# Performance work log

Measured on AMD Instinct MI355X. Metric: run time of the kernel, lower is better.

## Reference

```python
import jax, jax.numpy as jnp
import numpy as np

D_MODEL = 512; D_INNER = 1024; D_SSM = 512; D_STATE = 16; DT_RANK = 32; D_CONV = 4
BETA = 0.0; ALPHA = 1.0  # module defaults: no momentum -> vanilla Longhorn scan
B = 8; L = 2048


def dwconv_silu(x, w, b):
    # x: (B, C, L), w: (C, 1, K); torch F.conv1d(padding='same') with K=4 pads (left=1, right=2)
    y = jax.lax.conv_general_dilated(
        x, w, window_strides=(1,), padding=[(1, 2)],
        dimension_numbers=('NCH', 'OIH', 'NCH'), feature_group_count=x.shape[1])
    y = y + b[None, :, None]
    return y * jax.nn.sigmoid(y)


def longhorn_scan(u, q, k, dt, D_skip, t_bias):
    # u, dt: (B, D, L); q, k: (B, N, L). Longhorn online-learner SSM with momentum velocity.
    delta = jax.nn.softplus(dt + t_bias[None, :, None])           # (B, D, L)
    k2 = jnp.sum(k * k, axis=1, keepdims=True)                    # (B, 1, L)
    eps = delta / (1.0 + delta * k2)                              # implicit-update step size

    def step(carry, inp):
        S, v = carry                                              # (B, D, N) each
        eps_t, u_t, k_t, q_t = inp                                # (B,D),(B,D),(B,N),(B,N)
        g = eps_t[:, :, None] * (u_t[:, :, None] - S * k_t[:, None, :]) * k_t[:, None, :]
        v = BETA * v + ALPHA * g                                  # momentum velocity
        S = S + v
        y_t = jnp.einsum('bdn,bn->bd', S, q_t)
        return (S, v), y_t

    Bq, Dm, _ = u.shape
    S0 = jnp.zeros((Bq, Dm, q.shape[1]), u.dtype)
    xs = (jnp.moveaxis(eps, 2, 0), jnp.moveaxis(u, 2, 0),
          jnp.moveaxis(k, 2, 0), jnp.moveaxis(q, 2, 0))
    _, ys = jax.lax.scan(step, (S0, S0), xs)                      # ys: (L, B, D)
    return jnp.moveaxis(ys, 0, 2) + D_skip[None, :, None] * u    # (B, D, L)


def setup_inputs() -> dict:
    key = jax.random.key(0)
    ks = jax.random.split(key, 12)
    s = lambda k, shape, sc: jax.random.normal(k, shape, jnp.float32) * sc
    dt0 = jnp.exp(jax.random.uniform(ks[8], (D_SSM,), jnp.float32,
                                     float(np.log(1e-3)), float(np.log(1e-1))))
    b_dt = jnp.log(jnp.expm1(dt0))  # inv-softplus init as in torch module
    return {
        'hidden_states': s(ks[0], (B, L, D_MODEL), 1.0),
        'W_in': s(ks[1], (D_INNER, D_MODEL), 0.02),
        'conv_x_w': s(ks[2], (D_SSM, 1, D_CONV), 0.3),
        'conv_x_b': s(ks[3], (D_SSM,), 0.02),
        'conv_z_w': s(ks[4], (D_SSM, 1, D_CONV), 0.3),
        'conv_z_b': s(ks[5], (D_SSM,), 0.02),
        'W_xproj': s(ks[6], (DT_RANK + 2 * D_STATE, D_SSM), 0.05),
        'W_dt': s(ks[7], (D_SSM, DT_RANK), DT_RANK ** -0.5),
        'b_dt': b_dt,
        'D_skip': jnp.ones((D_SSM,), jnp.float32),
        'W_out': s(ks[9], (D_MODEL, D_INNER), 0.02),
    }


def reference(hidden_states, W_in, conv_x_w, conv_x_b, conv_z_w, conv_z_b,
              W_xproj, W_dt, b_dt, D_skip, W_out):
    xz = jnp.einsum('bld,ed->ble', hidden_states, W_in)           # (B, L, d_inner)
    xz = jnp.swapaxes(xz, 1, 2)                                   # (B, d_inner, L)
    x, z = xz[:, :D_SSM], xz[:, D_SSM:]
    x = dwconv_silu(x, conv_x_w, conv_x_b)
    z = dwconv_silu(z, conv_z_w, conv_z_b)
    x_dbl = jnp.einsum('bdl,ed->bel', x, W_xproj)                 # (B, r+2N, L)
    dt_low = x_dbl[:, :DT_RANK]
    k = x_dbl[:, DT_RANK:DT_RANK + D_STATE]
    q = x_dbl[:, DT_RANK + D_STATE:]
    dt = jnp.einsum('dr,brl->bdl', W_dt, dt_low)                  # (B, d_ssm, L)
    y = longhorn_scan(x, q, k, dt, D_skip, b_dt)                  # (B, d_ssm, L)
    y = jnp.concatenate([y, z], axis=1)                           # (B, d_inner, L)
    y = jnp.swapaxes(y, 1, 2)                                     # (B, L, d_inner)
    return jnp.einsum('ble,de->bld', y, W_out)                    # (B, L, d_model)
```

## Files before the change

kernel.cpp:

```cpp
#include <hip/hip_runtime.h>
#include <hip/hip_bf16.h>
#include <math.h>

#define BB 8
#define LL 2048
#define DMODEL 512
#define DINNER 1024
#define DSSM 512
#define NST 16
#define DTR 32
#define NXD 640
#define CCH 64
#define LC (LL / CCH)
#define BDN (BB * DSSM * NST)
#define CLW 8

typedef short short8 __attribute__((ext_vector_type(8)));
typedef float f32x4 __attribute__((ext_vector_type(4)));

__device__ __forceinline__ unsigned short f2bf(float f) {
  unsigned u = __float_as_uint(f);
  u += 0x7FFFu + ((u >> 16) & 1u);
  return (unsigned short)(u >> 16);
}
__device__ __forceinline__ float bf2f(unsigned short s) {
  return __uint_as_float(((unsigned)s) << 16);
}

__device__ __forceinline__ void gload16(const void* g, void* l) {
  __builtin_amdgcn_global_load_lds(
      (const __attribute__((address_space(1))) void*)g,
      (__attribute__((address_space(3))) void*)l, 16, 0, 0);
}

template<bool OUTBF>
__global__ __launch_bounds__(256) void gemm_bf16(
    const unsigned short* __restrict__ Ab,
    const unsigned short* __restrict__ Wb,
    void* __restrict__ Cout, int K, int NBN) {
  __shared__ unsigned short tA[128 * 64];
  __shared__ unsigned short tW[128 * 64];
  const int tid = threadIdx.x;
  const int ln = tid & 63;
  const int wv = tid >> 6;
  const int wr = wv >> 1, wc = wv & 1;
  const int lr = ln & 15, kc = ln >> 4;

  const int nwg = gridDim.x;
  const int q = nwg >> 3;
  const int bid = blockIdx.x;
  const int wg = (bid & 7) * q + (bid >> 3);
  const int mblk = wg / NBN, nblk = wg % NBN;
  const size_t m0 = (size_t)mblk * 128, n0 = (size_t)nblk * 128;

  f32x4 acc[4][4];
#pragma unroll
  for (int m = 0; m < 4; ++m)
#pragma unroll
    for (int n = 0; n < 4; ++n)
#pragma unroll
      for (int j = 0; j < 4; ++j) acc[m][n][j] = 0.f;

  const int wbase = (tid & 0xC0) << 4;

  for (int k0 = 0; k0 < K; k0 += 64) {
#pragma unroll
    for (int it = 0; it < 4; ++it) {
      const int gi = it * 256 + tid;
      const int r = gi >> 3, s = gi & 7, g = s ^ (r & 7);
      const size_t off = (m0 + r) * (size_t)K + (size_t)(k0 + g * 8);
      gload16(Ab + off, (char*)tA + it * 4096 + wbase);
    }
#pragma unroll
    for (int it = 0; it < 4; ++it) {
      const int gi = it * 256 + tid;
      const int r = gi >> 3, s = gi & 7, g = s ^ (r & 7);
      const size_t off = (n0 + r) * (size_t)K + (size_t)(k0 + g * 8);
      gload16(Wb + off, (char*)tW + it * 4096 + wbase);
    }
    __syncthreads();

    short8 alo[4], ahi[4], wlo[4], whi[4];
#pragma unroll
    for (int m = 0; m < 4; ++m) {
      const int ra = wr * 64 + m * 16 + lr;
      const int sl = kc ^ (ra & 7);
      const char* base = (const char*)tA + ra * 128;
      alo[m] = *(const short8*)(base + sl * 16);
      ahi[m] = *(const short8*)(base + (sl ^ 4) * 16);
    }
#pragma unroll
    for (int n = 0; n < 4; ++n) {
      const int rb = wc * 64 + n * 16 + lr;
      const int sl = kc ^ (rb & 7);
      const char* base = (const char*)tW + rb * 128;
      wlo[n] = *(const short8*)(base + sl * 16);
      whi[n] = *(const short8*)(base + (sl ^ 4) * 16);
    }
#pragma unroll
    for (int m = 0; m < 4; ++m)
#pragma unroll
      for (int n = 0; n < 4; ++n) {
        acc[m][n] = __builtin_amdgcn_mfma_f32_16x16x32_bf16(alo[m], wlo[n], acc[m][n], 0, 0, 0);
        acc[m][n] = __builtin_amdgcn_mfma_f32_16x16x32_bf16(ahi[m], whi[n], acc[m][n], 0, 0, 0);
      }
    __syncthreads();
  }

  const int ldc = NBN * 128;
#pragma unroll
  for (int m = 0; m < 4; ++m) {
    const size_t row0 = m0 + wr * 64 + m * 16 + kc * 4;
#pragma unroll
    for (int n = 0; n < 4; ++n) {
      const size_t col = n0 + wc * 64 + n * 16 + lr;
#pragma unroll
      for (int j = 0; j < 4; ++j) {
        if (OUTBF)
          ((unsigned short*)Cout)[(row0 + j) * (size_t)ldc + col] = f2bf(acc[m][n][j]);
        else
          ((float*)Cout)[(row0 + j) * (size_t)ldc + col] = acc[m][n][j];
      }
    }
  }
}

__global__ __launch_bounds__(256) void cvt_kernel(const float* __restrict__ in,
    unsigned short* __restrict__ o, int n4) {
  int i = blockIdx.x * 256 + threadIdx.x;
  const int str = gridDim.x * 256;
  for (; i < n4; i += str) {
    const float4 v = ((const float4*)in)[i];
    ushort4 h;
    h.x = f2bf(v.x); h.y = f2bf(v.y); h.z = f2bf(v.z); h.w = f2bf(v.w);
    ((ushort4*)o)[i] = h;
  }
}

__global__ __launch_bounds__(256) void weff_kernel(
    const float* __restrict__ W_dt, const float* __restrict__ W_xproj,
    unsigned short* __restrict__ WcatB) {
  const int c = blockIdx.x * 256 + threadIdx.x;
  const int r0 = blockIdx.y;
  float v;
  if (r0 < 512) {
    float acc = 0.f;
#pragma unroll
    for (int r = 0; r < 32; r++)
      acc = fmaf(W_dt[r0 * 32 + r], W_xproj[r * 512 + c], acc);
    v = acc;
  } else if (r0 < 544) {
    v = W_xproj[(r0 - 480) * 512 + c];
  } else {
    v = 0.f;
  }
  WcatB[(size_t)r0 * 512 + c] = f2bf(v);
}

__global__ __launch_bounds__(256) void conv_silu_kernel(
    const unsigned short* __restrict__ xzB,
    const float* __restrict__ cxw, const float* __restrict__ cxb,
    const float* __restrict__ czw, const float* __restrict__ czb,
    unsigned short* __restrict__ xcB, unsigned short* __restrict__ yB) {
  const int c = blockIdx.x * 256 + threadIdx.x;
  const int l0 = blockIdx.y * CLW;
  const int b = blockIdx.z;
  float w0, w1, w2, w3, bias;
  if (c < DSSM) {
    w0 = cxw[c * 4 + 0]; w1 = cxw[c * 4 + 1]; w2 = cxw[c * 4 + 2]; w3 = cxw[c * 4 + 3];
    bias = cxb[c];
  } else {
    const int cz = c - DSSM;
    w0 = czw[cz * 4 + 0]; w1 = czw[cz * 4 + 1]; w2 = czw[cz * 4 + 2]; w3 = czw[cz * 4 + 3];
    bias = czb[cz];
  }
  const unsigned short* base = xzB + ((size_t)b * LL + l0) * DINNER + c;
  float v[CLW + 3];
  v[0] = (l0 > 0) ? bf2f(base[-(int)DINNER]) : 0.f;
#pragma unroll
  for (int i = 0; i <= CLW + 1; i++) {
    const int l = l0 + i;
    v[i + 1] = (l < LL) ? bf2f(base[(size_t)i * DINNER]) : 0.f;
  }
#pragma unroll
  for (int j = 0; j < CLW; j++) {
    float a = bias;
    a = fmaf(v[j + 0], w0, a);
    a = fmaf(v[j + 1], w1, a);
    a = fmaf(v[j + 2], w2, a);
    a = fmaf(v[j + 3], w3, a);
    const float y = a / (1.f + expf(-a));
    const size_t bl = (size_t)b * LL + l0 + j;
    if (c < DSSM)
      xcB[bl * DSSM + c] = f2bf(y);
    else
      yB[bl * DINNER + c] = f2bf(y);
  }
}

__global__ __launch_bounds__(256) void dteps2_kernel(
    const float* __restrict__ xdbl2, const float* __restrict__ b_dt,
    float* __restrict__ eps) {
  const int half = blockIdx.x;
  const size_t row = blockIdx.y;
  const int d = half * 256 + threadIdx.x;
  const float* rp = xdbl2 + row * NXD;
  float k2 = 0.f;
#pragma unroll
  for (int n = 0; n < 16; n++) { const float kv = rp[512 + n]; k2 = fmaf(kv, kv, k2); }
  const float dt = rp[d] + b_dt[d];
  const float delta = (dt > 20.f) ? dt : log1pf(expf(dt));
  eps[row * DSSM + d] = delta / (1.f + delta * k2);
}

__global__ __launch_bounds__(256) void scan_passA(
    const float* __restrict__ eps, const unsigned short* __restrict__ xcB,
    const float* __restrict__ xdbl2,
    float* __restrict__ Ach, float* __restrict__ Bch) {
  const int d = blockIdx.x * 256 + threadIdx.x;
  const int b = blockIdx.y, ch = blockIdx.z;
  const size_t bl0 = (size_t)b * LL + (size_t)ch * LC;
  const float* ep = eps + bl0 * DSSM + d;
  const unsigned short* up = xcB + bl0 * DSSM + d;
  const float* kq = xdbl2 + bl0 * NXD + 512;
  float A[16], S[16];
#pragma unroll
  for (int n = 0; n < 16; n++) { A[n] = 1.f; S[n] = 0.f; }
#pragma unroll 2
  for (int j = 0; j < LC; j++) {
    const float e = ep[(size_t)j * DSSM];
    const float u = bf2f(up[(size_t)j * DSSM]);
    const float* kj = kq + j * NXD;
#pragma unroll
    for (int n = 0; n < 16; n++) {
      const float k = kj[n];
      const float t0 = e * k;
      const float a = fmaf(-t0, k, 1.f);
      A[n] *= a;
      S[n] = fmaf(S[n], a, t0 * u);
    }
  }
  const size_t base = (size_t)ch * BDN + (((size_t)b * DSSM + d) << 4);
#pragma unroll
  for (int n4 = 0; n4 < 4; n4++) {
    ((float4*)(Ach + base))[n4] =
        make_float4(A[4 * n4], A[4 * n4 + 1], A[4 * n4 + 2], A[4 * n4 + 3]);
    ((float4*)(Bch + base))[n4] =
        make_float4(S[4 * n4], S[4 * n4 + 1], S[4 * n4 + 2], S[4 * n4 + 3]);
  }
}

__global__ __launch_bounds__(256) void scan_passB(
    const float* __restrict__ Ach, const float* __restrict__ Bch,
    float* __restrict__ S0) {
  const size_t i = (size_t)blockIdx.x * 256 + threadIdx.x;
  float S = 0.f;
  for (int ch = 0; ch < CCH; ch++) {
    const size_t off = (size_t)ch * BDN + i;
    const float a = Ach[off];
    const float bv = Bch[off];
    S0[off] = S;
    S = fmaf(S, a, bv);
  }
}

__global__ __launch_bounds__(256) void scan_passC(
    const float* __restrict__ eps, const unsigned short* __restrict__ xcB,
    const float* __restrict__ xdbl2, const float* __restrict__ D_skip,
    const float* __restrict__ S0, unsigned short* __restrict__ yB) {
  const int d = blockIdx.x * 256 + threadIdx.x;
  const int b = blockIdx.y, ch = blockIdx.z;
  const size_t bl0 = (size_t)b * LL + (size_t)ch * LC;
  const float* ep = eps + bl0 * DSSM + d;
  const unsigned short* up = xcB + bl0 * DSSM + d;
  const float* kq = xdbl2 + bl0 * NXD + 512;
  unsigned short* yp = yB + bl0 * DINNER + d;
  const float Dv = D_skip[d];
  const size_t base = (size_t)ch * BDN + (((size_t)b * DSSM + d) << 4);
  float S[16];
#pragma unroll
  for (int n4 = 0; n4 < 4; n4++) {
    const float4 v = ((const float4*)(S0 + base))[n4];
    S[4 * n4 + 0] = v.x; S[4 * n4 + 1] = v.y;
    S[4 * n4 + 2] = v.z; S[4 * n4 + 3] = v.w;
  }
#pragma unroll 2
  for (int j = 0; j < LC; j++) {
    const float e = ep[(size_t)j * DSSM];
    const float u = bf2f(up[(size_t)j * DSSM]);
    const float* kj = kq + j * NXD;
#pragma unroll
    for (int n = 0; n < 16; n++) {
      const float k = kj[n];
      const float t0 = e * k;
      const float a = fmaf(-t0, k, 1.f);
      S[n] = fmaf(S[n], a, t0 * u);
    }
    float y0 = 0.f, y1 = 0.f, y2 = 0.f, y3 = 0.f;
#pragma unroll
    for (int n = 0; n < 16; n += 4) {
      y0 = fmaf(S[n + 0], kj[16 + n + 0], y0);
      y1 = fmaf(S[n + 1], kj[16 + n + 1], y1);
      y2 = fmaf(S[n + 2], kj[16 + n + 2], y2);
      y3 = fmaf(S[n + 3], kj[16 + n + 3], y3);
    }
    const float yv = fmaf(Dv, u, (y0 + y1) + (y2 + y3));
    yp[(size_t)j * DINNER] = f2bf(yv);
  }
}

extern "C" void kernel_launch(void* const* d_in, const int* in_sizes, int n_in,
                              void* d_out, int out_size, void* d_ws, size_t ws_size,
                              hipStream_t stream) {
  const float* hidden  = (const float*)d_in[0];
  const float* W_in    = (const float*)d_in[1];
  const float* cxw     = (const float*)d_in[2];
  const float* cxb     = (const float*)d_in[3];
  const float* czw     = (const float*)d_in[4];
  const float* czb     = (const float*)d_in[5];
  const float* W_xproj = (const float*)d_in[6];
  const float* W_dt    = (const float*)d_in[7];
  const float* b_dt    = (const float*)d_in[8];
  const float* D_skip  = (const float*)d_in[9];
  const float* W_out   = (const float*)d_in[10];
  float* out = (float*)d_out;

  const size_t ML  = (size_t)BB * LL;
  const size_t MK5 = ML * DSSM;
  const size_t MN  = ML * DINNER;
  const size_t WIN = (size_t)DINNER * DMODEL;
  const size_t WOU = (size_t)DMODEL * DINNER;
  const size_t WCT = (size_t)NXD * DMODEL;
  const size_t CB  = (size_t)CCH * BDN;

  unsigned short* WinB  = (unsigned short*)d_ws;
  unsigned short* WoutB = WinB + WIN;
  unsigned short* WcatB = WoutB + WOU;
  unsigned short* xcB   = WcatB + WCT;
  unsigned short* yB    = xcB + MK5;
  float* xdbl2 = (float*)(yB + MN);
  float* eps   = xdbl2 + ML * NXD;
  unsigned short* hidB = (unsigned short*)(eps + MK5);
  unsigned short* xzB  = hidB + MK5;
  float* Ach = (float*)hidB;
  float* Bch = Ach + CB;
  float* S0  = Bch + CB;

  cvt_kernel<<<2048, 256, 0, stream>>>(hidden, hidB, (int)(MK5 / 4));
  cvt_kernel<<<512, 256, 0, stream>>>(W_in, WinB, (int)(WIN / 4));
  cvt_kernel<<<512, 256, 0, stream>>>(W_out, WoutB, (int)(WOU / 4));
  weff_kernel<<<dim3(2, NXD), 256, 0, stream>>>(W_dt, W_xproj, WcatB);

  gemm_bf16<true><<<(16384 / 128) * (1024 / 128), 256, 0, stream>>>(
      hidB, WinB, xzB, DMODEL, DINNER / 128);

  conv_silu_kernel<<<dim3(DINNER / 256, LL / CLW, BB), 256, 0, stream>>>(
      xzB, cxw, cxb, czw, czb, xcB, yB);

  gemm_bf16<false><<<(16384 / 128) * (NXD / 128), 256, 0, stream>>>(
      xcB, WcatB, xdbl2, DMODEL, NXD / 128);

  dteps2_kernel<<<dim3(2, (unsigned)ML), 256, 0, stream>>>(xdbl2, b_dt, eps);

  scan_passA<<<dim3(2, BB, CCH), 256, 0, stream>>>(eps, xcB, xdbl2, Ach, Bch);
  scan_passB<<<dim3(BDN / 256), 256, 0, stream>>>(Ach, Bch, S0);
  scan_passC<<<dim3(2, BB, CCH), 256, 0, stream>>>(
      eps, xcB, xdbl2, D_skip, S0, yB);

  gemm_bf16<false><<<(16384 / 128) * (512 / 128), 256, 0, stream>>>(
      yB, WoutB, out, DINNER, DMODEL / 128);
}
```

Baseline: 286.8 us.

## Fuse dt/eps computation into scan passes and store xdbl in bf16

Removes the separate dteps2 kernel: both scan passes now recompute softplus(dt+b_dt) and the k-norm step size inline, reading dt, k and q from a bf16 copy of the x-projection output instead of fp32 xdbl2 plus an fp32 eps buffer. The x-projection GEMM now writes bf16 output. The three weight and activation conversion launches are merged into one prep kernel. This saves a launch and a large fp32 write/read of eps and halves xdbl traffic, at the cost of redundant transcendental math in both passes and reduced precision for dt, k and q.

```diff
diff --git a/kernel.cpp b/kernel.cpp
--- a/kernel.cpp
+++ b/kernel.cpp
@@ -125,10 +125,22 @@
   }
 }
 
-__global__ __launch_bounds__(256) void cvt_kernel(const float* __restrict__ in,
-    unsigned short* __restrict__ o, int n4) {
-  int i = blockIdx.x * 256 + threadIdx.x;
-  const int str = gridDim.x * 256;
+__global__ __launch_bounds__(256) void prep_kernel(
+    const float* __restrict__ hidden, const float* __restrict__ W_in,
+    const float* __restrict__ W_out,
+    unsigned short* __restrict__ hidB, unsigned short* __restrict__ WinB,
+    unsigned short* __restrict__ WoutB, int nHid4, int nW4) {
+  const int bx = blockIdx.x;
+  const float* in;
+  unsigned short* o;
+  int i, str, n4;
+  if (bx < 2048) {
+    in = hidden; o = hidB; i = bx * 256 + threadIdx.x; str = 2048 * 256; n4 = nHid4;
+  } else if (bx < 2176) {
+    in = W_in; o = WinB; i = (bx - 2048) * 256 + threadIdx.x; str = 128 * 256; n4 = nW4;
+  } else {
+    in = W_out; o = WoutB; i = (bx - 2176) * 256 + threadIdx.x; str = 128 * 256; n4 = nW4;
+  }
   for (; i < n4; i += str) {
     const float4 v = ((const float4*)in)[i];
     ushort4 h;
@@ -198,44 +210,44 @@
   }
 }
 
-__global__ __launch_bounds__(256) void dteps2_kernel(
-    const float* __restrict__ xdbl2, const float* __restrict__ b_dt,
-    float* __restrict__ eps) {
-  const int half = blockIdx.x;
-  const size_t row = blockIdx.y;
-  const int d = half * 256 + threadIdx.x;
-  const float* rp = xdbl2 + row * NXD;
-  float k2 = 0.f;
-#pragma unroll
-  for (int n = 0; n < 16; n++) { const float kv = rp[512 + n]; k2 = fmaf(kv, kv, k2); }
-  const float dt = rp[d] + b_dt[d];
-  const float delta = (dt > 20.f) ? dt : log1pf(expf(dt));
-  eps[row * DSSM + d] = delta / (1.f + delta * k2);
+__device__ __forceinline__ void load_bf16x16(const unsigned short* p, float* o) {
+  short8 lo = *(const short8*)p;
+  short8 hi = *(const short8*)(p + 8);
+#pragma unroll
+  for (int n = 0; n < 8; n++) o[n] = bf2f((unsigned short)lo[n]);
+#pragma unroll
+  for (int n = 0; n < 8; n++) o[8 + n] = bf2f((unsigned short)hi[n]);
 }
 
 __global__ __launch_bounds__(256) void scan_passA(
-    const float* __restrict__ eps, const unsigned short* __restrict__ xcB,
-    const float* __restrict__ xdbl2,
+    const unsigned short* __restrict__ xdbl2B,
+    const unsigned short* __restrict__ xcB, const float* __restrict__ b_dt,
     float* __restrict__ Ach, float* __restrict__ Bch) {
   const int d = blockIdx.x * 256 + threadIdx.x;
   const int b = blockIdx.y, ch = blockIdx.z;
   const size_t bl0 = (size_t)b * LL + (size_t)ch * LC;
-  const float* ep = eps + bl0 * DSSM + d;
+  const unsigned short* dtp = xdbl2B + bl0 * NXD + d;
   const unsigned short* up = xcB + bl0 * DSSM + d;
-  const float* kq = xdbl2 + bl0 * NXD + 512;
+  const unsigned short* kqp = xdbl2B + bl0 * NXD + 512;
+  const float bdt = b_dt[d];
   float A[16], S[16];
 #pragma unroll
   for (int n = 0; n < 16; n++) { A[n] = 1.f; S[n] = 0.f; }
 #pragma unroll 2
   for (int j = 0; j < LC; j++) {
-    const float e = ep[(size_t)j * DSSM];
+    float kv[16];
+    load_bf16x16(kqp + (size_t)j * NXD, kv);
+    float k2 = 0.f;
+#pragma unroll
+    for (int n = 0; n < 16; n++) k2 = fmaf(kv[n], kv[n], k2);
+    const float dt = bf2f(dtp[(size_t)j * NXD]) + bdt;
+    const float delta = (dt > 20.f) ? dt : log1pf(expf(dt));
+    const float e = delta / (1.f + delta * k2);
     const float u = bf2f(up[(size_t)j * DSSM]);
-    const float* kj = kq + j * NXD;
 #pragma unroll
     for (int n = 0; n < 16; n++) {
-      const float k = kj[n];
-      const float t0 = e * k;
-      const float a = fmaf(-t0, k, 1.f);
+      const float t0 = e * kv[n];
+      const float a = fmaf(-t0, kv[n], 1.f);
       A[n] *= a;
       S[n] = fmaf(S[n], a, t0 * u);
     }
@@ -265,16 +277,18 @@
 }
 
 __global__ __launch_bounds__(256) void scan_passC(
-    const float* __restrict__ eps, const unsigned short* __restrict__ xcB,
-    const float* __restrict__ xdbl2, const float* __restrict__ D_skip,
-    const float* __restrict__ S0, unsigned short* __restrict__ yB) {
+    const unsigned short* __restrict__ xdbl2B,
+    const unsigned short* __restrict__ xcB, const float* __restrict__ b_dt,
+    const float* __restrict__ D_skip, const float* __restrict__ S0,
+    unsigned short* __restrict__ yB) {
   const int d = blockIdx.x * 256 + threadIdx.x;
   const int b = blockIdx.y, ch = blockIdx.z;
   const size_t bl0 = (size_t)b * LL + (size_t)ch * LC;
-  const float* ep = eps + bl0 * DSSM + d;
+  const unsigned short* dtp = xdbl2B + bl0 * NXD + d;
   const unsigned short* up = xcB + bl0 * DSSM + d;
-  const float* kq = xdbl2 + bl0 * NXD + 512;
+  const unsigned short* kqp = xdbl2B + bl0 * NXD + 512;
   unsigned short* yp = yB + bl0 * DINNER + d;
+  const float bdt = b_dt[d];
   const float Dv = D_skip[d];
   const size_t base = (size_t)ch * BDN + (((size_t)b * DSSM + d) << 4);
   float S[16];
@@ -286,23 +300,29 @@
   }
 #pragma unroll 2
   for (int j = 0; j < LC; j++) {
-    const float e = ep[(size_t)j * DSSM];
+    float kv[16], qv[16];
+    load_bf16x16(kqp + (size_t)j * NXD, kv);
+    load_bf16x16(kqp + (size_t)j * NXD + 16, qv);
+    float k2 = 0.f;
+#pragma unroll
+    for (int n = 0; n < 16; n++) k2 = fmaf(kv[n], kv[n], k2);
+    const float dt = bf2f(dtp[(size_t)j * NXD]) + bdt;
+    const float delta = (dt > 20.f) ? dt : log1pf(expf(dt));
+    const float e = delta / (1.f + delta * k2);
     const float u = bf2f(up[(size_t)j * DSSM]);
-    const float* kj = kq + j * NXD;
-#pragma unroll
-    for (int n = 0; n < 16; n++) {
-      const float k = kj[n];
-      const float t0 = e * k;
-      const float a = fmaf(-t0, k, 1.f);
-      S[n] = fmaf(S[n], a, t0 * u);
-    }
     float y0 = 0.f, y1 = 0.f, y2 = 0.f, y3 = 0.f;
 #pragma unroll
     for (int n = 0; n < 16; n += 4) {
-      y0 = fmaf(S[n + 0], kj[16 + n + 0], y0);
-      y1 = fmaf(S[n + 1], kj[16 + n + 1], y1);
-      y2 = fmaf(S[n + 2], kj[16 + n + 2], y2);
-      y3 = fmaf(S[n + 3], kj[16 + n + 3], y3);
+      const float t00 = e * kv[n + 0], t01 = e * kv[n + 1];
+      const float t02 = e * kv[n + 2], t03 = e * kv[n + 3];
+      S[n + 0] = fmaf(S[n + 0], fmaf(-t00, kv[n + 0], 1.f), t00 * u);
+      S[n + 1] = fmaf(S[n + 1], fmaf(-t01, kv[n + 1], 1.f), t01 * u);
+      S[n + 2] = fmaf(S[n + 2], fmaf(-t02, kv[n + 2], 1.f), t02 * u);
+      S[n + 3] = fmaf(S[n + 3], fmaf(-t03, kv[n + 3], 1.f), t03 * u);
+      y0 = fmaf(S[n + 0], qv[n + 0], y0);
+      y1 = fmaf(S[n + 1], qv[n + 1], y1);
+      y2 = fmaf(S[n + 2], qv[n + 2], y2);
+      y3 = fmaf(S[n + 3], qv[n + 3], y3);
     }
     const float yv = fmaf(Dv, u, (y0 + y1) + (y2 + y3));
     yp[(size_t)j * DINNER] = f2bf(yv);
@@ -333,22 +353,20 @@
   const size_t WCT = (size_t)NXD * DMODEL;
   const size_t CB  = (size_t)CCH * BDN;
 
-  unsigned short* WinB  = (unsigned short*)d_ws;
-  unsigned short* WoutB = WinB + WIN;
-  unsigned short* WcatB = WoutB + WOU;
-  unsigned short* xcB   = WcatB + WCT;
-  unsigned short* yB    = xcB + MK5;
-  float* xdbl2 = (float*)(yB + MN);
-  float* eps   = xdbl2 + ML * NXD;
-  unsigned short* hidB = (unsigned short*)(eps + MK5);
-  unsigned short* xzB  = hidB + MK5;
+  unsigned short* WinB   = (unsigned short*)d_ws;
+  unsigned short* WoutB  = WinB + WIN;
+  unsigned short* WcatB  = WoutB + WOU;
+  unsigned short* xcB    = WcatB + WCT;
+  unsigned short* yB     = xcB + MK5;
+  unsigned short* xdbl2B = yB + MN;
+  unsigned short* hidB   = xdbl2B + ML * NXD;
+  unsigned short* xzB    = hidB + MK5;
   float* Ach = (float*)hidB;
   float* Bch = Ach + CB;
   float* S0  = Bch + CB;
 
-  cvt_kernel<<<2048, 256, 0, stream>>>(hidden, hidB, (int)(MK5 / 4));
-  cvt_kernel<<<512, 256, 0, stream>>>(W_in, WinB, (int)(WIN / 4));
-  cvt_kernel<<<512, 256, 0, stream>>>(W_out, WoutB, (int)(WOU / 4));
+  prep_kernel<<<2304, 256, 0, stream>>>(hidden, W_in, W_out, hidB, WinB, WoutB,
+                                        (int)(MK5 / 4), (int)(WIN / 4));
   weff_kernel<<<dim3(2, NXD), 256, 0, stream>>>(W_dt, W_xproj, WcatB);
 
   gemm_bf16<true><<<(16384 / 128) * (1024 / 128), 256, 0, stream>>>(
@@ -357,15 +375,13 @@
   conv_silu_kernel<<<dim3(DINNER / 256, LL / CLW, BB), 256, 0, stream>>>(
       xzB, cxw, cxb, czw, czb, xcB, yB);
 
-  gemm_bf16<false><<<(16384 / 128) * (NXD / 128), 256, 0, stream>>>(
-      xcB, WcatB, xdbl2, DMODEL, NXD / 128);
-
-  dteps2_kernel<<<dim3(2, (unsigned)ML), 256, 0, stream>>>(xdbl2, b_dt, eps);
-
-  scan_passA<<<dim3(2, BB, CCH), 256, 0, stream>>>(eps, xcB, xdbl2, Ach, Bch);
+  gemm_bf16<true><<<(16384 / 128) * (NXD / 128), 256, 0, stream>>>(
+      xcB, WcatB, xdbl2B, DMODEL, NXD / 128);
+
+  scan_passA<<<dim3(2, BB, CCH), 256, 0, stream>>>(xdbl2B, xcB, b_dt, Ach, Bch);
   scan_passB<<<dim3(BDN / 256), 256, 0, stream>>>(Ach, Bch, S0);
   scan_passC<<<dim3(2, BB, CCH), 256, 0, stream>>>(
-      eps, xcB, xdbl2, D_skip, S0, yB);
+      xdbl2B, xcB, b_dt, D_skip, S0, yB);
 
   gemm_bf16<false><<<(16384 / 128) * (512 / 128), 256, 0, stream>>>(
       yB, WoutB, out, DINNER, DMODEL / 128);
```

Result: slower. 308.2 us (+7.5%).
